# Kernel tuning notes

Measured on AMD Instinct MI355X. Metric: run time of the kernel, lower is better.

Reference implementation:

```python
import math
import jax, jax.numpy as jnp
import numpy as np

SIZE = 512
N_HEADS = 8
HEAD = SIZE // N_HEADS
SCALE = 1.0 / math.sqrt(HEAD)


def setup_inputs() -> dict:
    key = jax.random.key(0)
    ks = jax.random.split(key, 10)
    B, Sq, Skv = 4, 2048, 2048
    std = 1.0 / math.sqrt(SIZE)
    inp = {
        "query": jax.random.normal(ks[0], (B, Sq, SIZE), jnp.float32),
        "key_value": jax.random.normal(ks[1], (B, Skv, SIZE), jnp.float32),
        "Wq": jax.random.normal(ks[2], (SIZE, SIZE), jnp.float32) * std,
        "bq": jax.random.normal(ks[3], (SIZE,), jnp.float32) * std,
        "Wk": jax.random.normal(ks[4], (SIZE, SIZE), jnp.float32) * std,
        "bk": jax.random.normal(ks[5], (SIZE,), jnp.float32) * std,
        "Wv": jax.random.normal(ks[6], (SIZE, SIZE), jnp.float32) * std,
        "bv": jax.random.normal(ks[7], (SIZE,), jnp.float32) * std,
        "Wo": jax.random.normal(ks[8], (SIZE, SIZE), jnp.float32) * std,
        "bo": jax.random.normal(ks[9], (SIZE,), jnp.float32) * std,
    }
    return inp


def reference(query, key_value, Wq, bq, Wk, bk, Wv, bv, Wo, bo):
    B, Sq, D = query.shape
    Skv = key_value.shape[1]
    H, hd = N_HEADS, HEAD

    # Linear projections (torch nn.Linear: x @ W.T + b)
    q = query @ Wq.T + bq            # [B, Sq, D]
    k = key_value @ Wk.T + bk        # [B, Skv, D]
    v = key_value @ Wv.T + bv        # [B, Skv, D]

    # split heads: [B, S, H, hd]
    qh = q.reshape(B, Sq, H, hd)
    kh = k.reshape(B, Skv, H, hd)
    vh = v.reshape(B, Skv, H, hd)

    # attention scores and softmax over keys
    scores = jnp.einsum("bqhd,bkhd->bhqk", qh, kh) * SCALE  # [B, H, Sq, Skv]
    A = jax.nn.softmax(scores, axis=-1)
    o = jnp.einsum("bhqk,bkhd->bqhd", A, vh)                 # [B, Sq, H, hd]

    # residual with q heads (clean_path=False), merge heads
    out = (qh + o).reshape(B, Sq, D)

    # output residual + ReLU FFN stage
    out = out + jax.nn.relu(out @ Wo.T + bo)
    return out
```

## Files before the change

kernel.cpp:

```cpp
#include <hip/hip_runtime.h>
#include <hip/hip_bf16.h>

typedef __hip_bfloat16 bf16;
typedef __attribute__((ext_vector_type(4))) float f32x4;
typedef __attribute__((ext_vector_type(16))) float f32x16;
typedef __attribute__((ext_vector_type(8))) __bf16 bf16x8;

#define DEVI static __device__ __forceinline__

DEVI void gload_lds16(const void* g, void* l) {
  __builtin_amdgcn_global_load_lds(
      (const __attribute__((address_space(1))) void*)g,
      (__attribute__((address_space(3))) void*)l, 16, 0, 0);
}

DEVI unsigned pkbf(float a, float b) {
  union { __hip_bfloat162 h2; unsigned u; } t;
  t.h2.x = __float2bfloat16(a);
  t.h2.y = __float2bfloat16(b);
  return t.u;
}

union PK4 { bf16 h[4]; unsigned long long ll; };

DEVI unsigned long long pack4(float4 v) {
  PK4 u;
  u.h[0] = __float2bfloat16(v.x); u.h[1] = __float2bfloat16(v.y);
  u.h[2] = __float2bfloat16(v.z); u.h[3] = __float2bfloat16(v.w);
  return u.ll;
}

__global__ void cvt_all(const float* __restrict__ q, const float* __restrict__ kv,
                        const float* __restrict__ wq, const float* __restrict__ wk,
                        const float* __restrict__ wv, const float* __restrict__ wo,
                        bf16* __restrict__ oq, bf16* __restrict__ okv,
                        bf16* __restrict__ owq, bf16* __restrict__ owk,
                        bf16* __restrict__ owv, bf16* __restrict__ owo) {
  int bid = blockIdx.x;
  if (bid < 4096) {
    int i = bid * 256 + threadIdx.x;
    reinterpret_cast<unsigned long long*>(oq)[i]  = pack4(reinterpret_cast<const float4*>(q)[i]);
    reinterpret_cast<unsigned long long*>(okv)[i] = pack4(reinterpret_cast<const float4*>(kv)[i]);
  } else {
    int i = (bid - 4096) * 256 + threadIdx.x;
    reinterpret_cast<unsigned long long*>(owq)[i] = pack4(reinterpret_cast<const float4*>(wq)[i]);
    reinterpret_cast<unsigned long long*>(owk)[i] = pack4(reinterpret_cast<const float4*>(wk)[i]);
    reinterpret_cast<unsigned long long*>(owv)[i] = pack4(reinterpret_cast<const float4*>(wv)[i]);
    reinterpret_cast<unsigned long long*>(owo)[i] = pack4(reinterpret_cast<const float4*>(wo)[i]);
  }
}

__global__ __launch_bounds__(256) void gemm_zone(
    const bf16* __restrict__ qb, const bf16* __restrict__ kvb,
    const bf16* __restrict__ wqb, const bf16* __restrict__ wkb, const bf16* __restrict__ wvb,
    const float* __restrict__ bq, const float* __restrict__ bk, const float* __restrict__ bv,
    bf16* __restrict__ qp, bf16* __restrict__ kp, bf16* __restrict__ vT) {
  constexpr int K = 512;
  __shared__ __align__(16) char smem[49152];
  const int tid = threadIdx.x;
  const int wave = tid >> 6, lane = tid & 63;
  const int bid = blockIdx.x;
  const int wgid = (bid & 7) * 192 + (bid >> 3);
  const int bm = wgid / 12;
  const int rz = wgid % 12;
  const int zone = rz >> 2, bn = rz & 3;
  const bf16* A = zone ? kvb : qb;
  const bf16* W = (zone == 0) ? wqb : (zone == 1 ? wkb : wvb);
  const float* bias = (zone == 0) ? bq : (zone == 1 ? bk : bv);
  const int wm = (wave >> 1) * 32, wn = (wave & 1) * 64;
  const int srow8 = lane >> 3, sslot = lane & 7;

  f32x4 acc[2][4] = {};

  const bf16* ap[2];
  const bf16* wp[4];
  char* adst[2];
  char* bdst[4];
#pragma unroll
  for (int i = 0; i < 2; ++i) {
    int c = wave * 2 + i;
    int row = c * 8 + srow8;
    int gs = sslot ^ (row & 7);
    ap[i] = A + (long)(bm * 64 + row) * K + gs * 8;
    adst[i] = smem + c * 1024;
  }
#pragma unroll
  for (int i = 0; i < 4; ++i) {
    int c = wave * 4 + i;
    int row = c * 8 + srow8;
    int gs = sslot ^ (row & 7);
    wp[i] = W + (long)(bn * 128 + row) * K + gs * 8;
    bdst[i] = smem + 8192 + c * 1024;
  }

  int aoff[2][2], boff[2][4];
#pragma unroll
  for (int ks = 0; ks < 2; ++ks) {
#pragma unroll
    for (int f = 0; f < 2; ++f) {
      int r = f * 16 + (lane & 15);
      aoff[ks][f] = (wm + r) * 128 + (((ks * 4 + (lane >> 4)) ^ (r & 7)) << 4);
    }
#pragma unroll
    for (int f = 0; f < 4; ++f) {
      int r = f * 16 + (lane & 15);
      boff[ks][f] = (wn + r) * 128 + (((ks * 4 + (lane >> 4)) ^ (r & 7)) << 4);
    }
  }

#define ZSTAGE(BUF)                                                       \
  {                                                                       \
    _Pragma("unroll") for (int i = 0; i < 2; ++i) {                       \
      gload_lds16(ap[i], adst[i] + (BUF) * 24576);                        \
      ap[i] += 64;                                                        \
    }                                                                     \
    _Pragma("unroll") for (int i = 0; i < 4; ++i) {                       \
      gload_lds16(wp[i], bdst[i] + (BUF) * 24576);                        \
      wp[i] += 64;                                                        \
    }                                                                     \
  }

#define ZBODY(BUF, LAST)                                                  \
  {                                                                       \
    if (!(LAST)) {                                                        \
      ZSTAGE((BUF) ^ 1)                                                   \
      asm volatile("s_waitcnt vmcnt(6)" ::: "memory");                    \
    } else {                                                              \
      asm volatile("s_waitcnt vmcnt(0)" ::: "memory");                    \
    }                                                                     \
    asm volatile("s_barrier" ::: "memory");                               \
    const char* Asb = smem + (BUF) * 24576;                               \
    const char* Bsb = Asb + 8192;                                         \
    _Pragma("unroll") for (int ks = 0; ks < 2; ++ks) {                    \
      bf16x8 af[2], bfv[4];                                               \
      _Pragma("unroll") for (int f = 0; f < 2; ++f)                       \
        af[f] = *reinterpret_cast<const bf16x8*>(Asb + aoff[ks][f]);      \
      _Pragma("unroll") for (int f = 0; f < 4; ++f)                       \
        bfv[f] = *reinterpret_cast<const bf16x8*>(Bsb + boff[ks][f]);     \
      _Pragma("unroll") for (int mf = 0; mf < 2; ++mf)                    \
        _Pragma("unroll") for (int nf = 0; nf < 4; ++nf)                  \
          acc[mf][nf] = __builtin_amdgcn_mfma_f32_16x16x32_bf16(          \
              af[mf], bfv[nf], acc[mf][nf], 0, 0, 0);                     \
    }                                                                     \
    asm volatile("s_barrier" ::: "memory");                               \
  }

  ZSTAGE(0)
#pragma unroll 1
  for (int kt = 0; kt < 8; kt += 2) {
    ZBODY(0, false)
    ZBODY(1, kt + 1 == 7)
  }
#undef ZSTAGE
#undef ZBODY

#pragma unroll
  for (int nf = 0; nf < 4; ++nf) {
    int col = bn * 128 + wn + nf * 16 + (lane & 15);
    float bia = bias[col];
#pragma unroll
    for (int mf = 0; mf < 2; ++mf) {
      int row0 = bm * 64 + wm + mf * 16 + (lane >> 4) * 4;
      if (zone < 2) {
        bf16* Ob = zone ? kp : qp;
#pragma unroll
        for (int j = 0; j < 4; ++j)
          Ob[(long)(row0 + j) * 512 + col] = __float2bfloat16(acc[mf][nf][j] + bia);
      } else {
        int b = row0 >> 11, s0 = row0 & 2047;
        int h = col >> 6, d = col & 63;
        union { ushort4 s; unsigned short u[4]; } pk;
#pragma unroll
        for (int j = 0; j < 4; ++j) {
          bf16 hv = __float2bfloat16(acc[mf][nf][j] + bia);
          pk.u[j] = *reinterpret_cast<unsigned short*>(&hv);
        }
        *reinterpret_cast<ushort4*>(vT + ((long)((b * 8 + h) * 64 + d)) * 2048 + s0) = pk.s;
      }
    }
  }
}

__global__ __launch_bounds__(256) void gemm_ffn(
    const bf16* __restrict__ A, const bf16* __restrict__ W,
    const float* __restrict__ bias, float* __restrict__ Of) {
  constexpr int K = 512;
  __shared__ __align__(16) char smem[49152];
  const int tid = threadIdx.x;
  const int wave = tid >> 6, lane = tid & 63;
  const int bid = blockIdx.x;
  const int wgid = (bid & 7) * 64 + (bid >> 3);
  const int bm = wgid >> 2, bn = wgid & 3;
  const int wm = (wave >> 1) * 32, wn = (wave & 1) * 64;
  const int srow8 = lane >> 3, sslot = lane & 7;

  f32x4 acc[2][4] = {};

  const bf16* ap[2];
  const bf16* wp[4];
  char* adst[2];
  char* bdst[4];
#pragma unroll
  for (int i = 0; i < 2; ++i) {
    int c = wave * 2 + i;
    int row = c * 8 + srow8;
    int gs = sslot ^ (row & 7);
    ap[i] = A + (long)(bm * 64 + row) * K + gs * 8;
    adst[i] = smem + c * 1024;
  }
#pragma unroll
  for (int i = 0; i < 4; ++i) {
    int c = wave * 4 + i;
    int row = c * 8 + srow8;
    int gs = sslot ^ (row & 7);
    wp[i] = W + (long)(bn * 128 + row) * K + gs * 8;
    bdst[i] = smem + 8192 + c * 1024;
  }

  int aoff[2][2], boff[2][4];
#pragma unroll
  for (int ks = 0; ks < 2; ++ks) {
#pragma unroll
    for (int f = 0; f < 2; ++f) {
      int r = f * 16 + (lane & 15);
      aoff[ks][f] = (wm + r) * 128 + (((ks * 4 + (lane >> 4)) ^ (r & 7)) << 4);
    }
#pragma unroll
    for (int f = 0; f < 4; ++f) {
      int r = f * 16 + (lane & 15);
      boff[ks][f] = (wn + r) * 128 + (((ks * 4 + (lane >> 4)) ^ (r & 7)) << 4);
    }
  }

#define FSTAGE(BUF)                                                       \
  {                                                                       \
    _Pragma("unroll") for (int i = 0; i < 2; ++i) {                       \
      gload_lds16(ap[i], adst[i] + (BUF) * 24576);                        \
      ap[i] += 64;                                                        \
    }                                                                     \
    _Pragma("unroll") for (int i = 0; i < 4; ++i) {                       \
      gload_lds16(wp[i], bdst[i] + (BUF) * 24576);                        \
      wp[i] += 64;                                                        \
    }                                                                     \
  }

#define FBODY(BUF, LAST)                                                  \
  {                                                                       \
    if (!(LAST)) {                                                        \
      FSTAGE((BUF) ^ 1)                                                   \
      asm volatile("s_waitcnt vmcnt(6)" ::: "memory");                    \
    } else {                                                              \
      asm volatile("s_waitcnt vmcnt(0)" ::: "memory");                    \
    }                                                                     \
    asm volatile("s_barrier" ::: "memory");                               \
    const char* Asb = smem + (BUF) * 24576;                               \
    const char* Bsb = Asb + 8192;                                         \
    _Pragma("unroll") for (int ks = 0; ks < 2; ++ks) {                    \
      bf16x8 af[2], bfv[4];                                               \
      _Pragma("unroll") for (int f = 0; f < 2; ++f)                       \
        af[f] = *reinterpret_cast<const bf16x8*>(Asb + aoff[ks][f]);      \
      _Pragma("unroll") for (int f = 0; f < 4; ++f)                       \
        bfv[f] = *reinterpret_cast<const bf16x8*>(Bsb + boff[ks][f]);     \
      _Pragma("unroll") for (int mf = 0; mf < 2; ++mf)                    \
        _Pragma("unroll") for (int nf = 0; nf < 4; ++nf)                  \
          acc[mf][nf] = __builtin_amdgcn_mfma_f32_16x16x32_bf16(          \
              af[mf], bfv[nf], acc[mf][nf], 0, 0, 0);                     \
    }                                                                     \
    asm volatile("s_barrier" ::: "memory");                               \
  }

  FSTAGE(0)
#pragma unroll 1
  for (int kt = 0; kt < 8; kt += 2) {
    FBODY(0, false)
    FBODY(1, kt + 1 == 7)
  }
#undef FSTAGE
#undef FBODY

#pragma unroll
  for (int nf = 0; nf < 4; ++nf) {
    int col = bn * 128 + wn + nf * 16 + (lane & 15);
    float bia = bias[col];
#pragma unroll
    for (int mf = 0; mf < 2; ++mf) {
#pragma unroll
      for (int j = 0; j < 4; ++j) {
        int row = bm * 64 + wm + mf * 16 + (lane >> 4) * 4 + j;
        float r = __bfloat162float(A[(long)row * 512 + col]);
        Of[(long)row * 512 + col] = r + fmaxf(acc[mf][nf][j] + bia, 0.f);
      }
    }
  }
}

__global__ __launch_bounds__(256) void attn_k(
    const bf16* __restrict__ Q, const bf16* __restrict__ Kp,
    const bf16* __restrict__ VT, bf16* __restrict__ O) {
  __shared__ __align__(16) char smem[32768];
  const int tid = threadIdx.x, wave = tid >> 6, lane = tid & 63;
  const int bh = blockIdx.y, b = bh >> 3, h = bh & 7;
  const int q0 = blockIdx.x * 128 + wave * 32;
  const int ql = lane & 31, hl = lane >> 5;
  const long qg = ((long)(b * 2048 + q0 + ql)) * 512 + h * 64;
  const int srow8 = lane >> 3, sslot = lane & 7;

  bf16x8 qf[4];
#pragma unroll
  for (int c = 0; c < 4; ++c)
    qf[c] = *reinterpret_cast<const bf16x8*>(Q + qg + c * 16 + hl * 8);

  bf16x8 ones;
#pragma unroll
  for (int j = 0; j < 8; ++j) ones[j] = (__bf16)1.0f;

  f32x16 oacc[2] = {};
  f32x16 lacc = {};
  float m = -INFINITY;
  const float CEXP = 0.125f * 1.44269504088896f;

  const bf16* kgp[2];
  const bf16* vgp[2];
  char* kdst[2];
  char* vdst[2];
#pragma unroll
  for (int i = 0; i < 2; ++i) {
    int c = wave * 2 + i;
    int row = c * 8 + srow8;
    int gs = sslot ^ (row & 7);
    kgp[i] = Kp + ((long)(b * 2048 + row)) * 512 + h * 64 + gs * 8;
    vgp[i] = VT + ((long)(bh * 64 + row)) * 2048 + gs * 8;
    kdst[i] = smem + c * 1024;
    vdst[i] = smem + 8192 + c * 1024;
  }

  int ofs[2][4];
#pragma unroll
  for (int s = 0; s < 2; ++s)
#pragma unroll
    for (int c = 0; c < 4; ++c) {
      int row = s * 32 + ql;
      ofs[s][c] = row * 128 + (((c * 2 + hl) ^ (row & 7)) << 4);
    }

#define ASTAGE(BUF)                                                       \
  _Pragma("unroll") for (int i = 0; i < 2; ++i) {                         \
    gload_lds16(kgp[i], kdst[i] + (BUF) * 16384);                         \
    gload_lds16(vgp[i], vdst[i] + (BUF) * 16384);                         \
    kgp[i] += 32768; vgp[i] += 64;                                        \
  }

#define ABODY(BUF, LAST)                                                  \
  {                                                                       \
    if (!(LAST)) {                                                        \
      ASTAGE((BUF) ^ 1)                                                   \
      asm volatile("s_waitcnt vmcnt(4)" ::: "memory");                    \
    } else {                                                              \
      asm volatile("s_waitcnt vmcnt(0)" ::: "memory");                    \
    }                                                                     \
    asm volatile("s_barrier" ::: "memory");                               \
    const char* Kb = smem + (BUF) * 16384;                                \
    const char* Vb = Kb + 8192;                                           \
    f32x16 sacc[2] = {};                                                  \
    __builtin_amdgcn_s_setprio(1);                                        \
    _Pragma("unroll") for (int s = 0; s < 2; ++s)                         \
      _Pragma("unroll") for (int c = 0; c < 4; ++c) {                     \
        bf16x8 kf = *reinterpret_cast<const bf16x8*>(Kb + ofs[s][c]);     \
        sacc[s] = __builtin_amdgcn_mfma_f32_32x32x16_bf16(                \
            kf, qf[c], sacc[s], 0, 0, 0);                                 \
      }                                                                   \
    __builtin_amdgcn_s_setprio(0);                                        \
    float pmax = fmaxf(sacc[0][0], sacc[0][1]);                           \
    _Pragma("unroll") for (int i = 2; i < 16; i += 2)                     \
      pmax = fmaxf(fmaxf(pmax, sacc[0][i]), sacc[0][i + 1]);              \
    _Pragma("unroll") for (int i = 0; i < 16; i += 2)                     \
      pmax = fmaxf(fmaxf(pmax, sacc[1][i]), sacc[1][i + 1]);              \
    pmax = fmaxf(pmax, __shfl_xor(pmax, 32));                             \
    if (!__all(pmax - m <= 44.3614195558365f)) {                          \
      float mn = fmaxf(m, pmax);                                          \
      float al = exp2f((m - mn) * CEXP);                                  \
      m = mn;                                                             \
      _Pragma("unroll") for (int i = 0; i < 16; ++i) {                    \
        oacc[0][i] *= al; oacc[1][i] *= al; lacc[i] *= al;                \
      }                                                                   \
    }                                                                     \
    float nmC = -m * CEXP;                                                \
    float p[32];                                                          \
    _Pragma("unroll") for (int s = 0; s < 2; ++s)                         \
      _Pragma("unroll") for (int i = 0; i < 16; ++i)                      \
        p[s * 16 + i] = exp2f(fmaf(sacc[s][i], CEXP, nmC));               \
    __builtin_amdgcn_s_setprio(1);                                        \
    _Pragma("unroll") for (int s = 0; s < 2; ++s)                         \
      _Pragma("unroll") for (int jj = 0; jj < 2; ++jj) {                  \
        int base = s * 16 + jj * 8;                                       \
        unsigned w0 = pkbf(p[base + 0], p[base + 1]);                     \
        unsigned w1 = pkbf(p[base + 2], p[base + 3]);                     \
        unsigned w2 = pkbf(p[base + 4], p[base + 5]);                     \
        unsigned w3 = pkbf(p[base + 6], p[base + 7]);                     \
        asm("v_permlane32_swap_b32 %0, %1" : "+v"(w0), "+v"(w2));         \
        asm("v_permlane32_swap_b32 %0, %1" : "+v"(w1), "+v"(w3));         \
        union { unsigned u[4]; bf16x8 v; } pf;                            \
        pf.u[0] = w0; pf.u[1] = w1; pf.u[2] = w2; pf.u[3] = w3;           \
        lacc = __builtin_amdgcn_mfma_f32_32x32x16_bf16(                   \
            ones, pf.v, lacc, 0, 0, 0);                                   \
        int j = s * 2 + jj;                                               \
        _Pragma("unroll") for (int dblk = 0; dblk < 2; ++dblk) {          \
          bf16x8 vf = *reinterpret_cast<const bf16x8*>(Vb + ofs[dblk][j]);\
          oacc[dblk] = __builtin_amdgcn_mfma_f32_32x32x16_bf16(           \
              vf, pf.v, oacc[dblk], 0, 0, 0);                             \
        }                                                                 \
      }                                                                   \
    __builtin_amdgcn_s_setprio(0);                                        \
    asm volatile("s_barrier" ::: "memory");                               \
  }

  ASTAGE(0)
#pragma unroll 1
  for (int tt = 0; tt < 16; ++tt) {
    ABODY(0, false)
    ABODY(1, tt == 15)
  }
#undef ASTAGE
#undef ABODY

  float rl = 1.0f / lacc[0];
#pragma unroll
  for (int dblk = 0; dblk < 2; ++dblk) {
#pragma unroll
    for (int g = 0; g < 4; ++g) {
      int d0 = dblk * 32 + g * 8 + hl * 4;
      const long ga = qg + d0;
      union { ushort4 s; unsigned short u[4]; } qin, ov;
      qin.s = *reinterpret_cast<const ushort4*>(Q + ga);
#pragma unroll
      for (int i = 0; i < 4; ++i) {
        float qvf = __uint_as_float((unsigned)qin.u[i] << 16);
        float r = qvf + oacc[dblk][g * 4 + i] * rl;
        bf16 hb = __float2bfloat16(r);
        ov.u[i] = *reinterpret_cast<unsigned short*>(&hb);
      }
      *reinterpret_cast<ushort4*>(O + ga) = ov.s;
    }
  }
}

extern "C" void kernel_launch(void* const* d_in, const int* in_sizes, int n_in,
                              void* d_out, int out_size, void* d_ws, size_t ws_size,
                              hipStream_t stream) {
  const float* query = (const float*)d_in[0];
  const float* keyv  = (const float*)d_in[1];
  const float* Wq = (const float*)d_in[2];
  const float* bq = (const float*)d_in[3];
  const float* Wk = (const float*)d_in[4];
  const float* bk = (const float*)d_in[5];
  const float* Wv = (const float*)d_in[6];
  const float* bv = (const float*)d_in[7];
  const float* Wo = (const float*)d_in[8];
  const float* bo = (const float*)d_in[9];
  float* out = (float*)d_out;
  char* ws = (char*)d_ws;

  bf16* qb  = (bf16*)(ws + 0);
  bf16* kvb = (bf16*)(ws + 8388608);
  bf16* wqb = (bf16*)(ws + 16777216);
  bf16* wkb = (bf16*)(ws + 17301504);
  bf16* wvb = (bf16*)(ws + 17825792);
  bf16* wob = (bf16*)(ws + 18350080);
  bf16* qp  = (bf16*)(ws + 18874368);
  bf16* kp  = (bf16*)(ws + 27262976);
  bf16* vT  = (bf16*)(ws + 35651584);
  bf16* o1  = (bf16*)(ws + 44040192);

  cvt_all<<<4352, 256, 0, stream>>>(query, keyv, Wq, Wk, Wv, Wo,
                                    qb, kvb, wqb, wkb, wvb, wob);

  gemm_zone<<<1536, 256, 0, stream>>>(qb, kvb, wqb, wkb, wvb, bq, bk, bv, qp, kp, vT);

  attn_k<<<dim3(16, 32), 256, 0, stream>>>(qp, kp, vT, o1);

  gemm_ffn<<<512, 256, 0, stream>>>(o1, wob, bo, out);
}
```

Before: 194.4 us.

## Fuse fp32-to-bf16 conversion into projection GEMM tile loads and drop cvt kernel

Removes the separate conversion kernel and has the projection and FFN GEMMs read fp32 inputs and weights directly, converting to bf16 in registers before writing swizzled tiles to LDS. This saves a full extra pass writing and re-reading bf16 copies, plus one kernel launch. In exchange the GEMMs now read twice as many bytes per tile, fetch weight tiles repeatedly in fp32, and switch from async direct-to-LDS loads to register-staged loads with extra __syncthreads, which reduces load/compute overlap.

```diff
diff --git a/kernel.cpp b/kernel.cpp
--- a/kernel.cpp
+++ b/kernel.cpp
@@ -5,6 +5,7 @@
 typedef __attribute__((ext_vector_type(4))) float f32x4;
 typedef __attribute__((ext_vector_type(16))) float f32x16;
 typedef __attribute__((ext_vector_type(8))) __bf16 bf16x8;
+typedef __attribute__((ext_vector_type(8))) unsigned short u16x8;
 
 #define DEVI static __device__ __forceinline__
 
@@ -21,38 +22,18 @@
   return t.u;
 }
 
-union PK4 { bf16 h[4]; unsigned long long ll; };
-
-DEVI unsigned long long pack4(float4 v) {
-  PK4 u;
-  u.h[0] = __float2bfloat16(v.x); u.h[1] = __float2bfloat16(v.y);
-  u.h[2] = __float2bfloat16(v.z); u.h[3] = __float2bfloat16(v.w);
-  return u.ll;
-}
-
-__global__ void cvt_all(const float* __restrict__ q, const float* __restrict__ kv,
-                        const float* __restrict__ wq, const float* __restrict__ wk,
-                        const float* __restrict__ wv, const float* __restrict__ wo,
-                        bf16* __restrict__ oq, bf16* __restrict__ okv,
-                        bf16* __restrict__ owq, bf16* __restrict__ owk,
-                        bf16* __restrict__ owv, bf16* __restrict__ owo) {
-  int bid = blockIdx.x;
-  if (bid < 4096) {
-    int i = bid * 256 + threadIdx.x;
-    reinterpret_cast<unsigned long long*>(oq)[i]  = pack4(reinterpret_cast<const float4*>(q)[i]);
-    reinterpret_cast<unsigned long long*>(okv)[i] = pack4(reinterpret_cast<const float4*>(kv)[i]);
-  } else {
-    int i = (bid - 4096) * 256 + threadIdx.x;
-    reinterpret_cast<unsigned long long*>(owq)[i] = pack4(reinterpret_cast<const float4*>(wq)[i]);
-    reinterpret_cast<unsigned long long*>(owk)[i] = pack4(reinterpret_cast<const float4*>(wk)[i]);
-    reinterpret_cast<unsigned long long*>(owv)[i] = pack4(reinterpret_cast<const float4*>(wv)[i]);
-    reinterpret_cast<unsigned long long*>(owo)[i] = pack4(reinterpret_cast<const float4*>(wo)[i]);
-  }
+DEVI u16x8 cvt8(f32x4 a, f32x4 b) {
+  u16x8 r;
+#pragma unroll
+  for (int i = 0; i < 4; ++i) { bf16 h = __float2bfloat16(a[i]); r[i] = *reinterpret_cast<unsigned short*>(&h); }
+#pragma unroll
+  for (int i = 0; i < 4; ++i) { bf16 h = __float2bfloat16(b[i]); r[i + 4] = *reinterpret_cast<unsigned short*>(&h); }
+  return r;
 }
 
 __global__ __launch_bounds__(256) void gemm_zone(
-    const bf16* __restrict__ qb, const bf16* __restrict__ kvb,
-    const bf16* __restrict__ wqb, const bf16* __restrict__ wkb, const bf16* __restrict__ wvb,
+    const float* __restrict__ qf, const float* __restrict__ kvf,
+    const float* __restrict__ Wq, const float* __restrict__ Wk, const float* __restrict__ Wv,
     const float* __restrict__ bq, const float* __restrict__ bk, const float* __restrict__ bv,
     bf16* __restrict__ qp, bf16* __restrict__ kp, bf16* __restrict__ vT) {
   constexpr int K = 512;
@@ -64,33 +45,26 @@
   const int bm = wgid / 12;
   const int rz = wgid % 12;
   const int zone = rz >> 2, bn = rz & 3;
-  const bf16* A = zone ? kvb : qb;
-  const bf16* W = (zone == 0) ? wqb : (zone == 1 ? wkb : wvb);
+  const float* A = zone ? kvf : qf;
+  const float* W = (zone == 0) ? Wq : (zone == 1 ? Wk : Wv);
   const float* bias = (zone == 0) ? bq : (zone == 1 ? bk : bv);
   const int wm = (wave >> 1) * 32, wn = (wave & 1) * 64;
   const int srow8 = lane >> 3, sslot = lane & 7;
+  const int gs = sslot ^ srow8;
 
   f32x4 acc[2][4] = {};
 
-  const bf16* ap[2];
-  const bf16* wp[4];
-  char* adst[2];
-  char* bdst[4];
+  const float* afp[2];
+  const float* wfp[4];
 #pragma unroll
   for (int i = 0; i < 2; ++i) {
-    int c = wave * 2 + i;
-    int row = c * 8 + srow8;
-    int gs = sslot ^ (row & 7);
-    ap[i] = A + (long)(bm * 64 + row) * K + gs * 8;
-    adst[i] = smem + c * 1024;
+    int row = (wave * 2 + i) * 8 + srow8;
+    afp[i] = A + (long)(bm * 64 + row) * K + gs * 8;
   }
 #pragma unroll
   for (int i = 0; i < 4; ++i) {
-    int c = wave * 4 + i;
-    int row = c * 8 + srow8;
-    int gs = sslot ^ (row & 7);
-    wp[i] = W + (long)(bn * 128 + row) * K + gs * 8;
-    bdst[i] = smem + 8192 + c * 1024;
+    int row = (wave * 4 + i) * 8 + srow8;
+    wfp[i] = W + (long)(bn * 128 + row) * K + gs * 8;
   }
 
   int aoff[2][2], boff[2][4];
@@ -108,27 +82,34 @@
     }
   }
 
-#define ZSTAGE(BUF)                                                       \
+  f32x4 a0[2], a1[2], w0[4], w1[4];
+
+#define ZLOAD()                                                           \
   {                                                                       \
     _Pragma("unroll") for (int i = 0; i < 2; ++i) {                       \
-      gload_lds16(ap[i], adst[i] + (BUF) * 24576);                        \
-      ap[i] += 64;                                                        \
+      a0[i] = *reinterpret_cast<const f32x4*>(afp[i]);                    \
+      a1[i] = *reinterpret_cast<const f32x4*>(afp[i] + 4);                \
+      afp[i] += 64;                                                       \
     }                                                                     \
     _Pragma("unroll") for (int i = 0; i < 4; ++i) {                       \
-      gload_lds16(wp[i], bdst[i] + (BUF) * 24576);                        \
-      wp[i] += 64;                                                        \
-    }                                                                     \
-  }
-
-#define ZBODY(BUF, LAST)                                                  \
-  {                                                                       \
-    if (!(LAST)) {                                                        \
-      ZSTAGE((BUF) ^ 1)                                                   \
-      asm volatile("s_waitcnt vmcnt(6)" ::: "memory");                    \
-    } else {                                                              \
-      asm volatile("s_waitcnt vmcnt(0)" ::: "memory");                    \
-    }                                                                     \
-    asm volatile("s_barrier" ::: "memory");                               \
+      w0[i] = *reinterpret_cast<const f32x4*>(wfp[i]);                    \
+      w1[i] = *reinterpret_cast<const f32x4*>(wfp[i] + 4);                \
+      wfp[i] += 64;                                                       \
+    }                                                                     \
+  }
+
+#define ZWRITE(BUF)                                                       \
+  {                                                                       \
+    _Pragma("unroll") for (int i = 0; i < 2; ++i)                         \
+      *reinterpret_cast<u16x8*>(smem + (BUF) * 24576 +                    \
+          (wave * 2 + i) * 1024 + lane * 16) = cvt8(a0[i], a1[i]);        \
+    _Pragma("unroll") for (int i = 0; i < 4; ++i)                         \
+      *reinterpret_cast<u16x8*>(smem + (BUF) * 24576 + 8192 +             \
+          (wave * 4 + i) * 1024 + lane * 16) = cvt8(w0[i], w1[i]);        \
+  }
+
+#define ZCOMP(BUF)                                                        \
+  {                                                                       \
     const char* Asb = smem + (BUF) * 24576;                               \
     const char* Bsb = Asb + 8192;                                         \
     _Pragma("unroll") for (int ks = 0; ks < 2; ++ks) {                    \
@@ -142,17 +123,31 @@
           acc[mf][nf] = __builtin_amdgcn_mfma_f32_16x16x32_bf16(          \
               af[mf], bfv[nf], acc[mf][nf], 0, 0, 0);                     \
     }                                                                     \
-    asm volatile("s_barrier" ::: "memory");                               \
-  }
-
-  ZSTAGE(0)
+  }
+
+  ZLOAD()
+  ZWRITE(0)
+  __syncthreads();
 #pragma unroll 1
-  for (int kt = 0; kt < 8; kt += 2) {
-    ZBODY(0, false)
-    ZBODY(1, kt + 1 == 7)
-  }
-#undef ZSTAGE
-#undef ZBODY
+  for (int tt = 0; tt < 8; tt += 2) {
+    ZLOAD()
+    ZCOMP(0)
+    __syncthreads();
+    ZWRITE(1)
+    __syncthreads();
+    if (tt + 1 < 7) {
+      ZLOAD()
+      ZCOMP(1)
+      __syncthreads();
+      ZWRITE(0)
+      __syncthreads();
+    } else {
+      ZCOMP(1)
+    }
+  }
+#undef ZLOAD
+#undef ZWRITE
+#undef ZCOMP
 
 #pragma unroll
   for (int nf = 0; nf < 4; ++nf) {
@@ -182,7 +177,7 @@
 }
 
 __global__ __launch_bounds__(256) void gemm_ffn(
-    const bf16* __restrict__ A, const bf16* __restrict__ W,
+    const bf16* __restrict__ A, const float* __restrict__ W,
     const float* __restrict__ bias, float* __restrict__ Of) {
   constexpr int K = 512;
   __shared__ __align__(16) char smem[49152];
@@ -193,28 +188,21 @@
   const int bm = wgid >> 2, bn = wgid & 3;
   const int wm = (wave >> 1) * 32, wn = (wave & 1) * 64;
   const int srow8 = lane >> 3, sslot = lane & 7;
+  const int gs = sslot ^ srow8;
 
   f32x4 acc[2][4] = {};
 
-  const bf16* ap[2];
-  const bf16* wp[4];
-  char* adst[2];
-  char* bdst[4];
+  const bf16* abp[2];
+  const float* wfp[4];
 #pragma unroll
   for (int i = 0; i < 2; ++i) {
-    int c = wave * 2 + i;
-    int row = c * 8 + srow8;
-    int gs = sslot ^ (row & 7);
-    ap[i] = A + (long)(bm * 64 + row) * K + gs * 8;
-    adst[i] = smem + c * 1024;
+    int row = (wave * 2 + i) * 8 + srow8;
+    abp[i] = A + (long)(bm * 64 + row) * K + gs * 8;
   }
 #pragma unroll
   for (int i = 0; i < 4; ++i) {
-    int c = wave * 4 + i;
-    int row = c * 8 + srow8;
-    int gs = sslot ^ (row & 7);
-    wp[i] = W + (long)(bn * 128 + row) * K + gs * 8;
-    bdst[i] = smem + 8192 + c * 1024;
+    int row = (wave * 4 + i) * 8 + srow8;
+    wfp[i] = W + (long)(bn * 128 + row) * K + gs * 8;
   }
 
   int aoff[2][2], boff[2][4];
@@ -232,27 +220,34 @@
     }
   }
 
-#define FSTAGE(BUF)                                                       \
+  u16x8 areg[2];
+  f32x4 w0[4], w1[4];
+
+#define FLOAD()                                                           \
   {                                                                       \
     _Pragma("unroll") for (int i = 0; i < 2; ++i) {                       \
-      gload_lds16(ap[i], adst[i] + (BUF) * 24576);                        \
-      ap[i] += 64;                                                        \
+      areg[i] = *reinterpret_cast<const u16x8*>(abp[i]);                  \
+      abp[i] += 64;                                                       \
     }                                                                     \
     _Pragma("unroll") for (int i = 0; i < 4; ++i) {                       \
-      gload_lds16(wp[i], bdst[i] + (BUF) * 24576);                        \
-      wp[i] += 64;                                                        \
-    }                                                                     \
-  }
-
-#define FBODY(BUF, LAST)                                                  \
-  {                                                                       \
-    if (!(LAST)) {                                                        \
-      FSTAGE((BUF) ^ 1)                                                   \
-      asm volatile("s_waitcnt vmcnt(6)" ::: "memory");                    \
-    } else {                                                              \
-      asm volatile("s_waitcnt vmcnt(0)" ::: "memory");                    \
-    }                                                                     \
-    asm volatile("s_barrier" ::: "memory");                               \
+      w0[i] = *reinterpret_cast<const f32x4*>(wfp[i]);                    \
+      w1[i] = *reinterpret_cast<const f32x4*>(wfp[i] + 4);                \
+      wfp[i] += 64;                                                       \
+    }                                                                     \
+  }
+
+#define FWRITE(BUF)                                                       \
+  {                                                                       \
+    _Pragma("unroll") for (int i = 0; i < 2; ++i)                         \
+      *reinterpret_cast<u16x8*>(smem + (BUF) * 24576 +                    \
+          (wave * 2 + i) * 1024 + lane * 16) = areg[i];                   \
+    _Pragma("unroll") for (int i = 0; i < 4; ++i)                         \
+      *reinterpret_cast<u16x8*>(smem + (BUF) * 24576 + 8192 +             \
+          (wave * 4 + i) * 1024 + lane * 16) = cvt8(w0[i], w1[i]);        \
+  }
+
+#define FCOMP(BUF)                                                        \
+  {                                                                       \
     const char* Asb = smem + (BUF) * 24576;                               \
     const char* Bsb = Asb + 8192;                                         \
     _Pragma("unroll") for (int ks = 0; ks < 2; ++ks) {                    \
@@ -266,17 +261,31 @@
           acc[mf][nf] = __builtin_amdgcn_mfma_f32_16x16x32_bf16(          \
               af[mf], bfv[nf], acc[mf][nf], 0, 0, 0);                     \
     }                                                                     \
-    asm volatile("s_barrier" ::: "memory");                               \
-  }
-
-  FSTAGE(0)
+  }
+
+  FLOAD()
+  FWRITE(0)
+  __syncthreads();
 #pragma unroll 1
-  for (int kt = 0; kt < 8; kt += 2) {
-    FBODY(0, false)
-    FBODY(1, kt + 1 == 7)
-  }
-#undef FSTAGE
-#undef FBODY
+  for (int tt = 0; tt < 8; tt += 2) {
+    FLOAD()
+    FCOMP(0)
+    __syncthreads();
+    FWRITE(1)
+    __syncthreads();
+    if (tt + 1 < 7) {
+      FLOAD()
+      FCOMP(1)
+      __syncthreads();
+      FWRITE(0)
+      __syncthreads();
+    } else {
+      FCOMP(1)
+    }
+  }
+#undef FLOAD
+#undef FWRITE
+#undef FCOMP
 
 #pragma unroll
   for (int nf = 0; nf < 4; ++nf) {
@@ -460,23 +469,14 @@
   float* out = (float*)d_out;
   char* ws = (char*)d_ws;
 
-  bf16* qb  = (bf16*)(ws + 0);
-  bf16* kvb = (bf16*)(ws + 8388608);
-  bf16* wqb = (bf16*)(ws + 16777216);
-  bf16* wkb = (bf16*)(ws + 17301504);
-  bf16* wvb = (bf16*)(ws + 17825792);
-  bf16* wob = (bf16*)(ws + 18350080);
-  bf16* qp  = (bf16*)(ws + 18874368);
-  bf16* kp  = (bf16*)(ws + 27262976);
-  bf16* vT  = (bf16*)(ws + 35651584);
-  bf16* o1  = (bf16*)(ws + 44040192);
-
-  cvt_all<<<4352, 256, 0, stream>>>(query, keyv, Wq, Wk, Wv, Wo,
-                                    qb, kvb, wqb, wkb, wvb, wob);
-
-  gemm_zone<<<1536, 256, 0, stream>>>(qb, kvb, wqb, wkb, wvb, bq, bk, bv, qp, kp, vT);
+  bf16* qp = (bf16*)(ws + 18874368);
+  bf16* kp = (bf16*)(ws + 27262976);
+  bf16* vT = (bf16*)(ws + 35651584);
+  bf16* o1 = (bf16*)(ws + 44040192);
+
+  gemm_zone<<<1536, 256, 0, stream>>>(query, keyv, Wq, Wk, Wv, bq, bk, bv, qp, kp, vT);
 
   attn_k<<<dim3(16, 32), 256, 0, stream>>>(qp, kp, vT, o1);
 
-  gemm_ffn<<<512, 256, 0, stream>>>(o1, wob, bo, out);
-}
+  gemm_ffn<<<512, 256, 0, stream>>>(o1, Wo, bo, out);
+}
```

After: 202.1 us. 3.9% more time.
